# Kernel tuning notes

Measured on AMD Instinct MI355X. Metric: run time of the kernel, lower is better.

Reference implementation:

```python
import jax, jax.numpy as jnp
import numpy as np

N_NODES = 100000
N_EDGES = 800000
IN_DIM = 128
HID_DIM = 128


def setup_inputs() -> dict:
    key = jax.random.key(0)
    ks = jax.random.split(key, 10)
    s = 0.05
    return {
        "x": jax.random.normal(ks[0], (N_NODES, IN_DIM), dtype=jnp.float32),
        "edge_index": jax.random.randint(ks[1], (2, N_EDGES), 0, N_NODES, dtype=jnp.int64),
        "W1l": jax.random.normal(ks[2], (HID_DIM, IN_DIM), dtype=jnp.float32) * s,
        "b1": jax.random.normal(ks[3], (HID_DIM,), dtype=jnp.float32) * s,
        "W1r": jax.random.normal(ks[4], (HID_DIM, IN_DIM), dtype=jnp.float32) * s,
        "W2l": jax.random.normal(ks[5], (HID_DIM, HID_DIM), dtype=jnp.float32) * s,
        "b2": jax.random.normal(ks[6], (HID_DIM,), dtype=jnp.float32) * s,
        "W2r": jax.random.normal(ks[7], (HID_DIM, HID_DIM), dtype=jnp.float32) * s,
        "Wfc": jax.random.normal(ks[8], (1, HID_DIM), dtype=jnp.float32) * s,
        "bfc": jax.random.normal(ks[9], (1,), dtype=jnp.float32) * s,
    }


def _sage_conv(h, src, dst, n_nodes, Wl, b, Wr):
    # PyG SAGEConv (mean aggr): lin_l(mean_{j in N(i)} x_j) + lin_r(x_i)
    msg = h[src]  # [E, D] gather from source nodes
    agg = jax.ops.segment_sum(msg, dst, num_segments=n_nodes)  # [N, D]
    cnt = jax.ops.segment_sum(jnp.ones((src.shape[0], 1), h.dtype), dst,
                              num_segments=n_nodes)  # [N, 1]
    mean = agg / jnp.maximum(cnt, 1.0)  # isolated nodes -> 0 (matches scatter-mean)
    return mean @ Wl.T + b + h @ Wr.T


def reference(x, edge_index, W1l, b1, W1r, W2l, b2, W2r, Wfc, bfc):
    src, dst = edge_index[0], edge_index[1]
    n = x.shape[0]
    h = jax.nn.relu(_sage_conv(x, src, dst, n, W1l, b1, W1r))
    h = jax.nn.relu(_sage_conv(h, src, dst, n, W2l, b2, W2r))
    # dropout is identity in eval mode
    out = h @ Wfc.T + bfc  # [N, 1]
    return out.squeeze(-1)  # [N]
```

## Files before the change

kernel.cpp:

```cpp
#include <hip/hip_runtime.h>

#define N_NODES 100000
#define N_EDGES 800000
#define DIM 128

#define NB 391
#define BKCAP 2560
#define EPB 2048
#define BINB ((N_EDGES + EPB - 1) / EPB)
#define NXF (N_NODES * DIM / 4)
#define WF4 (4 * 4096)

typedef __attribute__((ext_vector_type(8))) short short8;
typedef __attribute__((ext_vector_type(4))) float float4v;
typedef __attribute__((ext_vector_type(2))) float float2v;
typedef __attribute__((ext_vector_type(4))) unsigned int uint4v;
typedef __attribute__((ext_vector_type(2))) unsigned int uint2v;

__device__ __forceinline__ float lo16(unsigned int v) {
    return __uint_as_float(v << 16);
}
__device__ __forceinline__ float hi16(unsigned int v) {
    return __uint_as_float(v & 0xffff0000u);
}
__device__ __forceinline__ float2v unp(unsigned int v) {
    return (float2v){lo16(v), hi16(v)};
}
__device__ __forceinline__ unsigned short f2bf(float f) {
    unsigned int x = __float_as_uint(f);
    unsigned int r = x + 0x7fffu + ((x >> 16) & 1u);
    return (unsigned short)(r >> 16);
}
__device__ __forceinline__ unsigned int packbf(float a, float b) {
    return (unsigned int)f2bf(a) | ((unsigned int)f2bf(b) << 16);
}

__device__ __forceinline__ int wave_iscan(int x, int lane) {
#pragma unroll
    for (int off = 1; off < 64; off <<= 1) {
        int n = __shfl_up(x, off, 64);
        x += (lane >= off) ? n : 0;
    }
    return x;
}


__device__ __forceinline__ void load_edge(const int* __restrict__ edge, int eflag, int e,
                                          int& s, int& d) {
    if (eflag == 0) {
        s = edge[2 * e];
        d = edge[2 * (N_EDGES + e)];
    } else {
        s = edge[e];
        d = edge[N_EDGES + e];
    }
}


__global__ __launch_bounds__(256) void binconv_kernel(
    const int* __restrict__ edge, int* __restrict__ cur,
    unsigned int* __restrict__ pairs, const float* __restrict__ x,
    const float* __restrict__ wa, const float* __restrict__ wb,
    const float* __restrict__ wc, const float* __restrict__ wd,
    unsigned int* __restrict__ xdst, unsigned int* __restrict__ wdst) {
    int t = threadIdx.x;
    if (blockIdx.x >= BINB) {
        int i = (blockIdx.x - BINB) * 256 + t;
        if (i < NXF) {
            float4 v = ((const float4*)x)[i];
            uint2v o = {packbf(v.x, v.y), packbf(v.z, v.w)};
            *(uint2v*)(xdst + 2 * (size_t)i) = o;
        } else {
            int j = i - NXF;
            if (j < WF4) {
                int m = j >> 12, r = j & 4095;
                const float* src = (m == 0) ? wa : (m == 1) ? wb : (m == 2) ? wc : wd;
                float4 v = ((const float4*)src)[r];
                uint2v o = {packbf(v.x, v.y), packbf(v.z, v.w)};
                *(uint2v*)(wdst + (size_t)m * 8192 + 2 * r) = o;
            }
        }
        return;
    }
    __shared__ int lcnt[NB];
    __shared__ int lbase[NB];
    for (int i = t; i < NB; i += 256) lcnt[i] = 0;
    int e0 = blockIdx.x * EPB;
    int eflag = __any(edge[2 * (e0 + t) + 1] != 0) ? 1 : 0;
    __syncthreads();
    int vb[8];
    unsigned int vp[8];
    bool valid[8];
#pragma unroll
    for (int k = 0; k < 8; ++k) {
        int e = e0 + k * 256 + t;
        valid[k] = false;
        if (e < N_EDGES) {
            int s, d;
            load_edge(edge, eflag, e, s, d);
            if ((unsigned)s < N_NODES && (unsigned)d < N_NODES) {
                valid[k] = true;
                vb[k] = d >> 8;
                vp[k] = ((unsigned int)s << 8) | (unsigned int)(d & 255);
                atomicAdd(&lcnt[vb[k]], 1);
            }
        }
    }
    __syncthreads();
    for (int i = t; i < NB; i += 256) {
        int c = lcnt[i];
        lbase[i] = (c > 0) ? atomicAdd(&cur[i], c) : 0;
        lcnt[i] = 0;
    }
    __syncthreads();
#pragma unroll
    for (int k = 0; k < 8; ++k) {
        if (valid[k]) {
            int b = vb[k];
            int pos = lbase[b] + atomicAdd(&lcnt[b], 1);
            if (pos < BKCAP)
                pairs[(size_t)b * BKCAP + pos] = vp[k];
        }
    }
}


__global__ __launch_bounds__(256) void csr_kernel(const int* __restrict__ cur,
                                                  const unsigned int* __restrict__ pairs,
                                                  int* __restrict__ rowptr,
                                                  int* __restrict__ esrc) {
    __shared__ int sh[512];
    __shared__ int hist[256];
    __shared__ int wsum[8];
    int b = blockIdx.x, t = threadIdx.x;
    int lane = t & 63, wv = t >> 6;
    int e0 = 2 * t, e1 = 2 * t + 1;
    int v0 = (e0 < NB) ? min(cur[e0], BKCAP) : 0;
    int v1 = (e1 < NB) ? min(cur[e1], BKCAP) : 0;
    int p = wave_iscan(v0 + v1, lane);
    if (lane == 63) wsum[wv] = p;
    hist[t] = 0;
    __syncthreads();
    int wpre = 0;
#pragma unroll
    for (int w = 0; w < 4; ++w) wpre += (w < wv) ? wsum[w] : 0;
    int incl1 = wpre + p;
    sh[e0] = incl1 - v1;
    sh[e1] = incl1;
    __syncthreads();
    int n = min(cur[b], BKCAP);
    int base = sh[b] - n;
    if (b == 0 && t == 0) rowptr[N_NODES] = sh[NB - 1];
    const unsigned int* pp = pairs + (size_t)b * BKCAP;
    for (int i = t; i < n; i += 256) atomicAdd(&hist[pp[i] & 255u], 1);
    __syncthreads();
    int v = hist[t];
    int ix = wave_iscan(v, lane);
    if (lane == 63) wsum[4 + wv] = ix;
    __syncthreads();
    int wpre2 = 0;
#pragma unroll
    for (int w = 0; w < 4; ++w) wpre2 += (w < wv) ? wsum[4 + w] : 0;
    int excl = wpre2 + ix - v;
    int node = b * 256 + t;
    if (node < N_NODES) rowptr[node] = base + excl;
    hist[t] = excl;
    __syncthreads();
    for (int i = t; i < n; i += 256) {
        unsigned int pk = pp[i];
        int pos = atomicAdd(&hist[pk & 255u], 1);
        esrc[base + pos] = (int)(pk >> 8);
    }
}


__global__ __launch_bounds__(256) void agg_kernel(const unsigned int* __restrict__ feat2,
                                                  const int* __restrict__ rowptr,
                                                  const int* __restrict__ esrc,
                                                  unsigned int* __restrict__ meanout) {
    int wid = (blockIdx.x * blockDim.x + threadIdx.x) >> 6;
    int lane = threadIdx.x & 63;
    int rowgrp = lane >> 4;
    int dimgrp = lane & 15;
    const int nwaves = 2048 * 4;
    int node = wid;
    int beg = rowptr[node], end = rowptr[node + 1];
    while (1) {
        int nn = node + nwaves;
        int nbg = 0, nen = 0;
        if (nn < N_NODES) {
            nbg = rowptr[nn];
            nen = rowptr[nn + 1];
        }
        float2v a0 = {0.f, 0.f}, a1 = {0.f, 0.f}, a2 = {0.f, 0.f}, a3 = {0.f, 0.f};
        int e = beg;
        for (; e + 8 <= end; e += 8) {
            int s0 = esrc[e + rowgrp];
            int s1 = esrc[e + 4 + rowgrp];
            uint4v v0 = *(const uint4v*)(feat2 + (size_t)s0 * 64 + dimgrp * 4);
            uint4v v1 = *(const uint4v*)(feat2 + (size_t)s1 * 64 + dimgrp * 4);
            a0 += unp(v0.x) + unp(v1.x);
            a1 += unp(v0.y) + unp(v1.y);
            a2 += unp(v0.z) + unp(v1.z);
            a3 += unp(v0.w) + unp(v1.w);
        }
        if (e < end) {
            int i0 = e + rowgrp, i1 = e + 4 + rowgrp;
            bool ok0 = i0 < end, ok1 = i1 < end;
            int s0 = esrc[ok0 ? i0 : end - 1];
            int s1 = esrc[ok1 ? i1 : end - 1];
            uint4v v0 = *(const uint4v*)(feat2 + (size_t)s0 * 64 + dimgrp * 4);
            uint4v v1 = *(const uint4v*)(feat2 + (size_t)s1 * 64 + dimgrp * 4);
            float m0 = ok0 ? 1.f : 0.f, m1 = ok1 ? 1.f : 0.f;
            float2v m0v = {m0, m0}, m1v = {m1, m1};
            a0 += m0v * unp(v0.x) + m1v * unp(v1.x);
            a1 += m0v * unp(v0.y) + m1v * unp(v1.y);
            a2 += m0v * unp(v0.z) + m1v * unp(v1.z);
            a3 += m0v * unp(v0.w) + m1v * unp(v1.w);
        }
        float2v s0v = (rowgrp & 1) ? a0 : a1;
        float2v k0v = (rowgrp & 1) ? a1 : a0;
        float2v s2v = (rowgrp & 1) ? a2 : a3;
        float2v k2v = (rowgrp & 1) ? a3 : a2;
        k0v.x += __shfl_xor(s0v.x, 16, 64);
        k0v.y += __shfl_xor(s0v.y, 16, 64);
        k2v.x += __shfl_xor(s2v.x, 16, 64);
        k2v.y += __shfl_xor(s2v.y, 16, 64);
        float2v sv = (rowgrp & 2) ? k0v : k2v;
        float2v kv = (rowgrp & 2) ? k2v : k0v;
        kv.x += __shfl_xor(sv.x, 32, 64);
        kv.y += __shfl_xor(sv.y, 32, 64);
        int deg = end - beg;
        float sc = deg > 0 ? 1.f / (float)deg : 0.f;
        meanout[(size_t)node * 64 + dimgrp * 4 + rowgrp] = packbf(kv.x * sc, kv.y * sc);
        if (nn >= N_NODES) break;
        node = nn;
        beg = nbg;
        end = nen;
    }
}


template <int FUSE_FC>
__global__ __launch_bounds__(256, 2) void gemm_kernel(
    const unsigned short* __restrict__ A0, const unsigned short* __restrict__ A1,
    const unsigned int* __restrict__ Wpk,
    const float* __restrict__ bias, const float* __restrict__ wfc,
    const float* __restrict__ bfc, unsigned short* __restrict__ hout,
    float* __restrict__ out) {
    __shared__ unsigned int wlds[16384];

    {
        int mat = threadIdx.x >> 7, row = threadIdx.x & 127;
        const unsigned int* g = Wpk + mat * 8192 + row * 64;
        unsigned int* lbase = wlds + mat * 8192;
#pragma unroll
        for (int q = 0; q < 16; ++q) {
            uint4v v = *(const uint4v*)(g + q * 4);
            *(uint4v*)(lbase + ((q * 128 + row) << 2)) = v;
        }
    }
    __syncthreads();

    int wave = threadIdx.x >> 6;
    int lane = threadIdx.x & 63;
    int lrow = lane & 15;
    int qsel = lane >> 4;
    int rowBase = blockIdx.x * 256 + wave * 64;

    float4v acc[4][8];
#pragma unroll
    for (int mt = 0; mt < 4; ++mt)
#pragma unroll
        for (int nt = 0; nt < 8; ++nt) acc[mt][nt] = (float4v){0.f, 0.f, 0.f, 0.f};

    const unsigned short* Ah[2] = {A0, A1};
    int r4a[4];
#pragma unroll
    for (int mt = 0; mt < 4; ++mt) {
        int r = rowBase + mt * 16 + lrow;
        r4a[mt] = (r >= N_NODES) ? (N_NODES - 1) : r;
    }

    short8 a[3][4];
#pragma unroll
    for (int mt = 0; mt < 4; ++mt) {
        a[0][mt] = *(const short8*)(A0 + (size_t)r4a[mt] * DIM + qsel * 8);
        a[1][mt] = *(const short8*)(A0 + (size_t)r4a[mt] * DIM + 32 + qsel * 8);
        a[2][mt] = *(const short8*)(A0 + (size_t)r4a[mt] * DIM + 64 + qsel * 8);
    }

#pragma unroll
    for (int step = 0; step < 8; ++step) {
        int half = step >> 2, kt = step & 3;
        int slot = step % 3;
        short8 cur[4];
#pragma unroll
        for (int mt = 0; mt < 4; ++mt) cur[mt] = a[slot][mt];
        if (step < 5) {
            int ns = step + 3;
            int nk0 = (ns & 3) * 32 + qsel * 8;
            const unsigned short* A = Ah[ns >> 2];
#pragma unroll
            for (int mt = 0; mt < 4; ++mt)
                a[slot][mt] = *(const short8*)(A + (size_t)r4a[mt] * DIM + nk0);
        }
        const unsigned int* lbase = wlds + half * 8192;
        int qg = kt * 4 + qsel;
#pragma unroll
        for (int nt = 0; nt < 8; ++nt) {
            short8 b = *(const short8*)(lbase + ((qg * 128 + nt * 16 + lrow) << 2));
#pragma unroll
            for (int mt = 0; mt < 4; ++mt)
                acc[mt][nt] = __builtin_amdgcn_mfma_f32_16x16x32_bf16(cur[mt], b, acc[mt][nt], 0, 0, 0);
        }
    }

    int crow0 = (lane >> 4) * 4;
    if (!FUSE_FC) {
#pragma unroll
        for (int mt = 0; mt < 4; ++mt) {
#pragma unroll
            for (int nt = 0; nt < 8; ++nt) {
                int col = nt * 16 + lrow;
                float bv = bias[col];
#pragma unroll
                for (int r4 = 0; r4 < 4; ++r4) {
                    int row = rowBase + mt * 16 + crow0 + r4;
                    if (row < N_NODES) {
                        float v = acc[mt][nt][r4] + bv;
                        hout[(size_t)row * DIM + col] = f2bf(v > 0.f ? v : 0.f);
                    }
                }
            }
        }
    } else {
        float bv[8], wv[8];
#pragma unroll
        for (int nt = 0; nt < 8; ++nt) {
            bv[nt] = bias[nt * 16 + lrow];
            wv[nt] = wfc[nt * 16 + lrow];
        }
        float bf0 = bfc[0];
#pragma unroll
        for (int mt = 0; mt < 4; ++mt) {
#pragma unroll
            for (int r4 = 0; r4 < 4; ++r4) {
                float p = 0.f;
#pragma unroll
                for (int nt = 0; nt < 8; ++nt) {
                    float v = acc[mt][nt][r4] + bv[nt];
                    p += (v > 0.f ? v : 0.f) * wv[nt];
                }
#pragma unroll
                for (int off = 1; off < 16; off <<= 1) p += __shfl_xor(p, off, 64);
                int row = rowBase + mt * 16 + crow0 + r4;
                if (lrow == 0 && row < N_NODES) out[row] = p + bf0;
            }
        }
    }
}


extern "C" void kernel_launch(void* const* d_in, const int* in_sizes, int n_in,
                              void* d_out, int out_size, void* d_ws, size_t ws_size,
                              hipStream_t stream) {
    const float* x  = (const float*)d_in[0];
    const int* edge = (const int*)d_in[1];
    const float* W1l = (const float*)d_in[2];
    const float* b1  = (const float*)d_in[3];
    const float* W1r = (const float*)d_in[4];
    const float* W2l = (const float*)d_in[5];
    const float* b2  = (const float*)d_in[6];
    const float* W2r = (const float*)d_in[7];
    const float* Wfc = (const float*)d_in[8];
    const float* bfc = (const float*)d_in[9];
    float* out = (float*)d_out;

    char* ws = (char*)d_ws;
    size_t off = 0;
    int* rowptr = (int*)(ws + off); off += ((size_t)N_NODES + 64) * 4;
    int* esrc   = (int*)(ws + off); off += (size_t)N_EDGES * 4;
    int* cur    = (int*)(ws + off); off += (size_t)NB * 4 + 256;
    off = (off + 255) & ~(size_t)255;
    unsigned int* pairs = (unsigned int*)(ws + off); off += (size_t)NB * BKCAP * 4;
    off = (off + 255) & ~(size_t)255;
    unsigned int* wbf = (unsigned int*)(ws + off); off += 4 * 8192 * 4;
    off = (off + 255) & ~(size_t)255;
    unsigned short* xbf  = (unsigned short*)(ws + off); off += (size_t)N_NODES * DIM * 2;
    unsigned short* mean = (unsigned short*)(ws + off); off += (size_t)N_NODES * DIM * 2;
    unsigned short* h1   = (unsigned short*)(ws + off); off += (size_t)N_NODES * DIM * 2;

    const int gemmBlocks = (N_NODES + 255) / 256;
    const int convBlocks = (NXF + WF4 + 255) / 256;

    hipMemsetAsync(cur, 0, NB * sizeof(int), stream);
    binconv_kernel<<<BINB + convBlocks, 256, 0, stream>>>(edge, cur, pairs, x,
                                                          W1l, W1r, W2l, W2r,
                                                          (unsigned int*)xbf, wbf);
    csr_kernel<<<NB, 256, 0, stream>>>(cur, pairs, rowptr, esrc);

    agg_kernel<<<2048, 256, 0, stream>>>((const unsigned int*)xbf, rowptr, esrc,
                                         (unsigned int*)mean);
    gemm_kernel<0><<<gemmBlocks, 256, 0, stream>>>(mean, xbf, wbf, b1, nullptr, nullptr,
                                                   h1, nullptr);
    agg_kernel<<<2048, 256, 0, stream>>>((const unsigned int*)h1, rowptr, esrc,
                                         (unsigned int*)mean);
    gemm_kernel<1><<<gemmBlocks, 256, 0, stream>>>(mean, h1, wbf + 2 * 8192, b2, Wfc, bfc,
                                                   nullptr, out);
}
```

Baseline: 239.7 us.

## Fuse neighbor mean aggregation with SAGE GEMM via shared-memory tile

Replaces the separate aggregation and GEMM kernels with one kernel per layer. Each 512-thread block aggregates 128 nodes into a swizzled LDS tile, then runs the MFMA GEMM against Wl and Wr, loading the two weight halves into LDS one after the other. This removes the global round-trip of the mean buffer and two kernel launches. In exchange it loses the persistent grid-stride load balancing and the prefetch of the next row pointers, and adds an extra weight reload and barriers per block.

```diff
diff --git a/kernel.cpp b/kernel.cpp
--- a/kernel.cpp
+++ b/kernel.cpp
@@ -10,6 +10,7 @@
 #define BINB ((N_EDGES + EPB - 1) / EPB)
 #define NXF (N_NODES * DIM / 4)
 #define WF4 (4 * 4096)
+#define NBLK ((N_NODES + 127) / 128)
 
 typedef __attribute__((ext_vector_type(8))) short short8;
 typedef __attribute__((ext_vector_type(4))) float float4v;
@@ -174,24 +175,39 @@
 }
 
 
-__global__ __launch_bounds__(256) void agg_kernel(const unsigned int* __restrict__ feat2,
-                                                  const int* __restrict__ rowptr,
-                                                  const int* __restrict__ esrc,
-                                                  unsigned int* __restrict__ meanout) {
-    int wid = (blockIdx.x * blockDim.x + threadIdx.x) >> 6;
-    int lane = threadIdx.x & 63;
+template <int FUSE_FC>
+__global__ __launch_bounds__(512, 4) void fused_kernel(
+    const unsigned int* __restrict__ feat2,
+    const unsigned short* __restrict__ A1g,
+    const int* __restrict__ rowptr, const int* __restrict__ esrc,
+    const unsigned int* __restrict__ Wpk,
+    const float* __restrict__ bias, const float* __restrict__ wfc,
+    const float* __restrict__ bfc, unsigned short* __restrict__ hout,
+    float* __restrict__ out) {
+    __shared__ unsigned int wlds[8192];
+    __shared__ unsigned int mlds[8192];
+
+    int t = threadIdx.x;
+    int wave = t >> 6, lane = t & 63;
     int rowgrp = lane >> 4;
     int dimgrp = lane & 15;
-    const int nwaves = 2048 * 4;
-    int node = wid;
-    int beg = rowptr[node], end = rowptr[node + 1];
-    while (1) {
-        int nn = node + nwaves;
-        int nbg = 0, nen = 0;
-        if (nn < N_NODES) {
-            nbg = rowptr[nn];
-            nen = rowptr[nn + 1];
-        }
+    int blockRow = blockIdx.x * 128;
+
+    {
+        int row = t >> 2, qb = (t & 3) << 2;
+        const unsigned int* g = Wpk + row * 64 + (qb << 2);
+#pragma unroll
+        for (int q = 0; q < 4; ++q) {
+            uint4v v = *(const uint4v*)(g + (q << 2));
+            *(uint4v*)(wlds + (((qb + q) * 128 + row) << 2)) = v;
+        }
+    }
+
+#pragma unroll 1
+    for (int i = 0; i < 16; ++i) {
+        int node = blockRow + wave * 16 + i;
+        if (node >= N_NODES) break;
+        int beg = rowptr[node], end = rowptr[node + 1];
         float2v a0 = {0.f, 0.f}, a1 = {0.f, 0.f}, a2 = {0.f, 0.f}, a3 = {0.f, 0.f};
         int e = beg;
         for (; e + 8 <= end; e += 8) {
@@ -232,105 +248,70 @@
         kv.y += __shfl_xor(sv.y, 32, 64);
         int deg = end - beg;
         float sc = deg > 0 ? 1.f / (float)deg : 0.f;
-        meanout[(size_t)node * 64 + dimgrp * 4 + rowgrp] = packbf(kv.x * sc, kv.y * sc);
-        if (nn >= N_NODES) break;
-        node = nn;
-        beg = nbg;
-        end = nen;
-    }
-}
-
-
-template <int FUSE_FC>
-__global__ __launch_bounds__(256, 2) void gemm_kernel(
-    const unsigned short* __restrict__ A0, const unsigned short* __restrict__ A1,
-    const unsigned int* __restrict__ Wpk,
-    const float* __restrict__ bias, const float* __restrict__ wfc,
-    const float* __restrict__ bfc, unsigned short* __restrict__ hout,
-    float* __restrict__ out) {
-    __shared__ unsigned int wlds[16384];
-
+        int r = wave * 16 + i;
+        mlds[r * 64 + ((dimgrp ^ (r & 15)) << 2) + rowgrp] = packbf(kv.x * sc, kv.y * sc);
+    }
+
+    int rA = blockRow + wave * 16 + dimgrp;
+    if (rA >= N_NODES) rA = N_NODES - 1;
+    short8 aA1[4];
+#pragma unroll
+    for (int kt = 0; kt < 4; ++kt)
+        aA1[kt] = *(const short8*)(A1g + (size_t)rA * DIM + kt * 32 + rowgrp * 8);
+
+    __syncthreads();
+
+    int lrow = dimgrp, qsel = rowgrp;
+    float4v acc[8];
+#pragma unroll
+    for (int nt = 0; nt < 8; ++nt) acc[nt] = (float4v){0.f, 0.f, 0.f, 0.f};
+
+    const unsigned int* mrow = mlds + (wave * 16 + lrow) * 64;
+#pragma unroll
+    for (int kt = 0; kt < 4; ++kt) {
+        short8 afr = *(const short8*)(mrow + (((kt * 4 + qsel) ^ lrow) << 2));
+        int qg = kt * 4 + qsel;
+#pragma unroll
+        for (int nt = 0; nt < 8; ++nt) {
+            short8 b = *(const short8*)(wlds + ((qg * 128 + nt * 16 + lrow) << 2));
+            acc[nt] = __builtin_amdgcn_mfma_f32_16x16x32_bf16(afr, b, acc[nt], 0, 0, 0);
+        }
+    }
+
+    __syncthreads();
     {
-        int mat = threadIdx.x >> 7, row = threadIdx.x & 127;
-        const unsigned int* g = Wpk + mat * 8192 + row * 64;
-        unsigned int* lbase = wlds + mat * 8192;
-#pragma unroll
-        for (int q = 0; q < 16; ++q) {
-            uint4v v = *(const uint4v*)(g + q * 4);
-            *(uint4v*)(lbase + ((q * 128 + row) << 2)) = v;
-        }
-    }
-    __syncthreads();
-
-    int wave = threadIdx.x >> 6;
-    int lane = threadIdx.x & 63;
-    int lrow = lane & 15;
-    int qsel = lane >> 4;
-    int rowBase = blockIdx.x * 256 + wave * 64;
-
-    float4v acc[4][8];
-#pragma unroll
-    for (int mt = 0; mt < 4; ++mt)
-#pragma unroll
-        for (int nt = 0; nt < 8; ++nt) acc[mt][nt] = (float4v){0.f, 0.f, 0.f, 0.f};
-
-    const unsigned short* Ah[2] = {A0, A1};
-    int r4a[4];
-#pragma unroll
-    for (int mt = 0; mt < 4; ++mt) {
-        int r = rowBase + mt * 16 + lrow;
-        r4a[mt] = (r >= N_NODES) ? (N_NODES - 1) : r;
-    }
-
-    short8 a[3][4];
-#pragma unroll
-    for (int mt = 0; mt < 4; ++mt) {
-        a[0][mt] = *(const short8*)(A0 + (size_t)r4a[mt] * DIM + qsel * 8);
-        a[1][mt] = *(const short8*)(A0 + (size_t)r4a[mt] * DIM + 32 + qsel * 8);
-        a[2][mt] = *(const short8*)(A0 + (size_t)r4a[mt] * DIM + 64 + qsel * 8);
-    }
-
-#pragma unroll
-    for (int step = 0; step < 8; ++step) {
-        int half = step >> 2, kt = step & 3;
-        int slot = step % 3;
-        short8 cur[4];
-#pragma unroll
-        for (int mt = 0; mt < 4; ++mt) cur[mt] = a[slot][mt];
-        if (step < 5) {
-            int ns = step + 3;
-            int nk0 = (ns & 3) * 32 + qsel * 8;
-            const unsigned short* A = Ah[ns >> 2];
-#pragma unroll
-            for (int mt = 0; mt < 4; ++mt)
-                a[slot][mt] = *(const short8*)(A + (size_t)r4a[mt] * DIM + nk0);
-        }
-        const unsigned int* lbase = wlds + half * 8192;
+        int row = t >> 2, qb = (t & 3) << 2;
+        const unsigned int* g = Wpk + 8192 + row * 64 + (qb << 2);
+#pragma unroll
+        for (int q = 0; q < 4; ++q) {
+            uint4v v = *(const uint4v*)(g + (q << 2));
+            *(uint4v*)(wlds + (((qb + q) * 128 + row) << 2)) = v;
+        }
+    }
+    __syncthreads();
+
+#pragma unroll
+    for (int kt = 0; kt < 4; ++kt) {
         int qg = kt * 4 + qsel;
 #pragma unroll
         for (int nt = 0; nt < 8; ++nt) {
-            short8 b = *(const short8*)(lbase + ((qg * 128 + nt * 16 + lrow) << 2));
-#pragma unroll
-            for (int mt = 0; mt < 4; ++mt)
-                acc[mt][nt] = __builtin_amdgcn_mfma_f32_16x16x32_bf16(cur[mt], b, acc[mt][nt], 0, 0, 0);
-        }
-    }
-
-    int crow0 = (lane >> 4) * 4;
+            short8 b = *(const short8*)(wlds + ((qg * 128 + nt * 16 + lrow) << 2));
+            acc[nt] = __builtin_amdgcn_mfma_f32_16x16x32_bf16(aA1[kt], b, acc[nt], 0, 0, 0);
+        }
+    }
+
+    int crow0 = qsel * 4;
     if (!FUSE_FC) {
 #pragma unroll
-        for (int mt = 0; mt < 4; ++mt) {
-#pragma unroll
-            for (int nt = 0; nt < 8; ++nt) {
-                int col = nt * 16 + lrow;
-                float bv = bias[col];
-#pragma unroll
-                for (int r4 = 0; r4 < 4; ++r4) {
-                    int row = rowBase + mt * 16 + crow0 + r4;
-                    if (row < N_NODES) {
-                        float v = acc[mt][nt][r4] + bv;
-                        hout[(size_t)row * DIM + col] = f2bf(v > 0.f ? v : 0.f);
-                    }
+        for (int nt = 0; nt < 8; ++nt) {
+            int col = nt * 16 + lrow;
+            float bv = bias[col];
+#pragma unroll
+            for (int r4 = 0; r4 < 4; ++r4) {
+                int row = blockRow + wave * 16 + crow0 + r4;
+                if (row < N_NODES) {
+                    float v = acc[nt][r4] + bv;
+                    hout[(size_t)row * DIM + col] = f2bf(v > 0.f ? v : 0.f);
                 }
             }
         }
@@ -343,20 +324,17 @@
         }
         float bf0 = bfc[0];
 #pragma unroll
-        for (int mt = 0; mt < 4; ++mt) {
-#pragma unroll
-            for (int r4 = 0; r4 < 4; ++r4) {
-                float p = 0.f;
-#pragma unroll
-                for (int nt = 0; nt < 8; ++nt) {
-                    float v = acc[mt][nt][r4] + bv[nt];
-                    p += (v > 0.f ? v : 0.f) * wv[nt];
-                }
-#pragma unroll
-                for (int off = 1; off < 16; off <<= 1) p += __shfl_xor(p, off, 64);
-                int row = rowBase + mt * 16 + crow0 + r4;
-                if (lrow == 0 && row < N_NODES) out[row] = p + bf0;
+        for (int r4 = 0; r4 < 4; ++r4) {
+            float p = 0.f;
+#pragma unroll
+            for (int nt = 0; nt < 8; ++nt) {
+                float v = acc[nt][r4] + bv[nt];
+                p += (v > 0.f ? v : 0.f) * wv[nt];
             }
+#pragma unroll
+            for (int off = 1; off < 16; off <<= 1) p += __shfl_xor(p, off, 64);
+            int row = blockRow + wave * 16 + crow0 + r4;
+            if (lrow == 0 && row < N_NODES) out[row] = p + bf0;
         }
     }
 }
@@ -387,11 +365,9 @@
     off = (off + 255) & ~(size_t)255;
     unsigned int* wbf = (unsigned int*)(ws + off); off += 4 * 8192 * 4;
     off = (off + 255) & ~(size_t)255;
-    unsigned short* xbf  = (unsigned short*)(ws + off); off += (size_t)N_NODES * DIM * 2;
-    unsigned short* mean = (unsigned short*)(ws + off); off += (size_t)N_NODES * DIM * 2;
-    unsigned short* h1   = (unsigned short*)(ws + off); off += (size_t)N_NODES * DIM * 2;
-
-    const int gemmBlocks = (N_NODES + 255) / 256;
+    unsigned short* xbf = (unsigned short*)(ws + off); off += (size_t)N_NODES * DIM * 2;
+    unsigned short* h1  = (unsigned short*)(ws + off); off += (size_t)N_NODES * DIM * 2;
+
     const int convBlocks = (NXF + WF4 + 255) / 256;
 
     hipMemsetAsync(cur, 0, NB * sizeof(int), stream);
@@ -400,12 +376,10 @@
                                                           (unsigned int*)xbf, wbf);
     csr_kernel<<<NB, 256, 0, stream>>>(cur, pairs, rowptr, esrc);
 
-    agg_kernel<<<2048, 256, 0, stream>>>((const unsigned int*)xbf, rowptr, esrc,
-                                         (unsigned int*)mean);
-    gemm_kernel<0><<<gemmBlocks, 256, 0, stream>>>(mean, xbf, wbf, b1, nullptr, nullptr,
-                                                   h1, nullptr);
-    agg_kernel<<<2048, 256, 0, stream>>>((const unsigned int*)h1, rowptr, esrc,
-                                         (unsigned int*)mean);
-    gemm_kernel<1><<<gemmBlocks, 256, 0, stream>>>(mean, h1, wbf + 2 * 8192, b2, Wfc, bfc,
-                                                   nullptr, out);
-}
+    fused_kernel<0><<<NBLK, 512, 0, stream>>>((const unsigned int*)xbf, xbf, rowptr,
+                                              esrc, wbf, b1, nullptr, nullptr, h1,
+                                              nullptr);
+    fused_kernel<1><<<NBLK, 512, 0, stream>>>((const unsigned int*)h1, h1, rowptr,
+                                              esrc, wbf + 2 * 8192, b2, Wfc, bfc,
+                                              nullptr, out);
+}
```

After: 269.6 us. 1.12x slower.
